# Optimization experiments

Hardware: AMD Instinct MI355X
Metric: run time of the kernel (lower is better)

The kernel has to match this reference:

```python
import jax, jax.numpy as jnp
import numpy as np

ELEM, EMBD = 512, 512

def setup_inputs() -> dict:
    key = jax.random.key(0)
    ks = jax.random.split(key, 7)
    s = 1.0 / np.sqrt(ELEM)
    return {
        "x": jax.random.normal(ks[0], (8, 2048, ELEM), dtype=jnp.float32),
        "Wq": jax.random.normal(ks[1], (ELEM, EMBD), dtype=jnp.float32) * s,
        "bq": jnp.zeros((EMBD,), dtype=jnp.float32),
        "Wk": jax.random.normal(ks[2], (ELEM, EMBD), dtype=jnp.float32) * s,
        "bk": jnp.zeros((EMBD,), dtype=jnp.float32),
        "Wv": jax.random.normal(ks[3], (ELEM, EMBD), dtype=jnp.float32) * s,
        "bv": jnp.zeros((EMBD,), dtype=jnp.float32),
    }

def reference(x, Wq, bq, Wk, bk, Wv, bv):
    # x: [N, S, E]
    q = x @ Wq + bq            # [N, S, D]
    k = x @ Wk + bk            # [N, S, D]
    v = x @ Wv + bv            # [N, S, D]
    # NOTE: original has no 1/sqrt(d) scaling.
    logits = jnp.einsum('nsd,ntd->nst', q, k)   # [N, S, S]
    attn = jax.nn.softmax(logits, axis=-1)
    return jnp.einsum('nst,ntd->nsd', attn, v)  # [N, S, D]
```

## Files before the change

kernel.cpp:

```cpp
#include <hip/hip_runtime.h>
#include <hip/hip_fp16.h>

#define SEQ 2048
#define DIM 512

typedef __attribute__((ext_vector_type(8))) short short8;
typedef __attribute__((ext_vector_type(4))) float f32x4;
typedef _Float16 h8 __attribute__((ext_vector_type(8)));
typedef _Float16 h4 __attribute__((ext_vector_type(4)));

#define MFMA16(a, b, c) __builtin_amdgcn_mfma_f32_16x16x32_f16((a), (b), (c), 0, 0, 0)

#define GLOAD_LDS16(g, l)                                                              \
    __builtin_amdgcn_global_load_lds(                                                  \
        (const __attribute__((address_space(1))) unsigned int*)(g),                    \
        (__attribute__((address_space(3))) unsigned int*)(l), 16, 0, 0)

template <int MODE>
__global__ __launch_bounds__(512, 1) void gemmw(
    const _Float16* __restrict__ A, const _Float16* __restrict__ B,
    const float* __restrict__ biasA, const float* __restrict__ biasB,
    _Float16* __restrict__ o0, _Float16* __restrict__ ovt) {
    extern __shared__ char sm[];
    constexpr int T  = (MODE == 0) ? 16 : 8;
    constexpr int PA = 512;
    constexpr int PB = (MODE == 0) ? 1024 : 512;

    int tid = threadIdx.x, wid = tid >> 6, lane = tid & 63, r = lane & 15, g = lane >> 4;
    int wm = wid >> 1, wn = wid & 1;
    int m0 = blockIdx.x * 256, n0 = blockIdx.y * 128;

    const _Float16* Ab = A + (size_t)m0 * 512;
    const _Float16* Bb = B + (size_t)n0 * PB;

    const char* gA[4];
    const char* gB[2];
    int ldsA[4], ldsB[2];
#pragma unroll
    for (int j = 0; j < 4; ++j) {
        int ci = j * 512 + tid;
        int row = ci >> 3, cl = ci & 7;
        int col16 = cl ^ (row & 7);
        gA[j] = (const char*)Ab + (size_t)row * (PA * 2) + col16 * 16;
        ldsA[j] = ci * 16;
    }
#pragma unroll
    for (int j = 0; j < 2; ++j) {
        int ci = j * 512 + tid;
        int row = ci >> 3, cl = ci & 7;
        int col16 = cl ^ (row & 7);
        gB[j] = (const char*)Bb + (size_t)row * (PB * 2) + col16 * 16;
        ldsB[j] = ci * 16;
    }
    int offA[4][2], offB[4][2];
#pragma unroll
    for (int m = 0; m < 4; ++m) {
        int rowA = wm * 64 + m * 16 + r;
        int rowB = wn * 64 + m * 16 + r;
#pragma unroll
        for (int ks = 0; ks < 2; ++ks) {
            offA[m][ks] = rowA * 128 + (((ks * 4 + g) ^ (rowA & 7)) * 16);
            offB[m][ks] = rowB * 128 + (((ks * 4 + g) ^ (rowB & 7)) * 16);
        }
    }

    f32x4 acc[4][4];
#pragma unroll
    for (int m = 0; m < 4; ++m)
#pragma unroll
        for (int n = 0; n < 4; ++n) acc[m][n] = (f32x4)(0.0f);

    auto STG = [&](int t, int b) {
        int ka = (MODE == 0) ? ((t & 7) * 128) : (t * 128);
        int kb = t * 128;
        char* dA = sm + b * 49152;
        char* dB = sm + b * 49152 + 32768;
#pragma unroll
        for (int j = 0; j < 4; ++j) GLOAD_LDS16(gA[j] + ka, dA + ldsA[j]);
#pragma unroll
        for (int j = 0; j < 2; ++j) GLOAD_LDS16(gB[j] + kb, dB + ldsB[j]);
    };

    STG(0, 0);
    STG(1, 1);
    asm volatile("s_waitcnt vmcnt(6)" ::: "memory");
    __builtin_amdgcn_s_barrier();

#pragma unroll
    for (int t = 0; t < T; ++t) {
        const int buf = t % 3;
        if (t + 2 < T) STG(t + 2, (t + 2) % 3);
        const char* bA = sm + buf * 49152;
        const char* bB = sm + buf * 49152 + 32768;
        h8 af[4][2], bf[4][2];
#pragma unroll
        for (int m = 0; m < 4; ++m)
#pragma unroll
            for (int ks = 0; ks < 2; ++ks) {
                af[m][ks] = *(const h8*)(bA + offA[m][ks]);
                bf[m][ks] = *(const h8*)(bB + offB[m][ks]);
            }
        __builtin_amdgcn_s_setprio(1);
#pragma unroll
        for (int ks = 0; ks < 2; ++ks)
#pragma unroll
            for (int m = 0; m < 4; ++m)
#pragma unroll
                for (int n = 0; n < 4; ++n)
                    acc[m][n] = MFMA16(af[m][ks], bf[n][ks], acc[m][n]);
        __builtin_amdgcn_s_setprio(0);
        if (t + 2 < T) asm volatile("s_waitcnt vmcnt(6)" ::: "memory");
        else if (t + 1 < T) asm volatile("s_waitcnt vmcnt(0)" ::: "memory");
        if (t + 1 < T) __builtin_amdgcn_s_barrier();
    }

    if (MODE == 0) {
#pragma unroll
        for (int n = 0; n < 4; ++n) {
            int col = n0 + wn * 64 + n * 16 + r;
            float bi = biasA[col];
#pragma unroll
            for (int m = 0; m < 4; ++m) {
                int grow0 = m0 + wm * 64 + m * 16 + 4 * g;
                for (int reg = 0; reg < 4; ++reg)
                    o0[(size_t)(grow0 + reg) * 512 + col] =
                        (_Float16)(acc[m][n][reg] + bi);
            }
        }
    } else {
        int p = n0 >> 9, ncl = n0 & 511;
        if (p == 0) {
#pragma unroll
            for (int n = 0; n < 4; ++n) {
                int col = ncl + wn * 64 + n * 16 + r;
                float bi = biasA[col];
#pragma unroll
                for (int m = 0; m < 4; ++m) {
                    int grow0 = m0 + wm * 64 + m * 16 + 4 * g;
                    for (int reg = 0; reg < 4; ++reg)
                        o0[(size_t)(grow0 + reg) * 512 + col] =
                            (_Float16)(acc[m][n][reg] + bi);
                }
            }
        } else {
            __syncthreads();
            _Float16* tt = (_Float16*)sm;
#pragma unroll
            for (int n = 0; n < 4; ++n) {
                int dloc = wn * 64 + n * 16 + r;
                float bi = biasB[ncl + dloc];
#pragma unroll
                for (int m = 0; m < 4; ++m) {
                    int sloc = wm * 64 + m * 16 + 4 * g;
                    h4 pv;
                    pv[0] = (_Float16)(acc[m][n][0] + bi);
                    pv[1] = (_Float16)(acc[m][n][1] + bi);
                    pv[2] = (_Float16)(acc[m][n][2] + bi);
                    pv[3] = (_Float16)(acc[m][n][3] + bi);
                    *(h4*)(&tt[dloc * 264 + sloc]) = pv;
                }
            }
            __syncthreads();
            int b = m0 >> 11, s0b = m0 & 2047;
            int drow = tid >> 2, part = tid & 3;
            const char* src = (const char*)(tt + drow * 264 + part * 64);
            char* dst = (char*)(ovt + (size_t)b * (512 * 2048) +
                                (size_t)(ncl + drow) * 2048 + s0b + part * 64);
#pragma unroll
            for (int j = 0; j < 8; ++j)
                *(short8*)(dst + j * 16) = *(const short8*)(src + j * 16);
        }
    }
}

template <int MODE>
__global__ __launch_bounds__(256) void gemmn(
    const _Float16* __restrict__ A, const _Float16* __restrict__ B,
    float* __restrict__ of, int bat0) {
    __shared__ char sm[2 * 32768];
    constexpr int T  = (MODE == 1) ? 8 : 32;
    constexpr int PA = (MODE == 1) ? 512 : 4096;
    constexpr int PB = (MODE == 1) ? 512 : 2048;

    int tid = threadIdx.x, wid = tid >> 6, lane = tid & 63, r = lane & 15, g = lane >> 4;
    int mw = wid >> 1, nw = wid & 1;
    int m0 = blockIdx.x * 128, n0 = blockIdx.y * 128, bz = blockIdx.z;

    const _Float16 *Ab, *Bb;
    if (MODE == 1) {
        int b = bat0 + bz;
        Ab = A + ((size_t)(b * SEQ) + m0) * 512;
        Bb = B + ((size_t)(b * SEQ) + n0) * 512;
    } else {
        int b = bat0 + bz;
        Ab = A + (size_t)bz * (SEQ * 4096) + (size_t)m0 * 4096;
        Bb = B + (size_t)b * (512 * SEQ) + (size_t)n0 * 2048;
    }

    const char* gA[4];
    const char* gB[4];
    int ldsw[4];
#pragma unroll
    for (int j = 0; j < 4; ++j) {
        int ci = (j * 4 + wid) * 64 + lane;
        int row = ci >> 3, cl = ci & 7;
        int col16 = cl ^ (row & 7);
        gA[j] = (const char*)Ab + (size_t)row * (PA * 2) + col16 * 16;
        gB[j] = (const char*)Bb + (size_t)row * (PB * 2) + col16 * 16;
        ldsw[j] = (j * 4 + wid) * 1024;
    }
    int offA[4][2], offB[4][2];
#pragma unroll
    for (int m = 0; m < 4; ++m) {
        int rowA = mw * 64 + m * 16 + r;
        int rowB = nw * 64 + m * 16 + r;
#pragma unroll
        for (int ks = 0; ks < 2; ++ks) {
            offA[m][ks] = rowA * 128 + (((ks * 4 + g) ^ (rowA & 7)) * 16);
            offB[m][ks] = rowB * 128 + (((ks * 4 + g) ^ (rowB & 7)) * 16);
        }
    }

    f32x4 acc[4][4];
#pragma unroll
    for (int m = 0; m < 4; ++m)
#pragma unroll
        for (int n = 0; n < 4; ++n) acc[m][n] = (f32x4)(0.0f);

    auto STG = [&](int t, int b) {
        int ka = t * 128, kb = t * 128;
        char* dA = sm + b * 32768;
        char* dB = sm + b * 32768 + 16384;
#pragma unroll
        for (int j = 0; j < 4; ++j) {
            GLOAD_LDS16(gA[j] + ka, dA + ldsw[j]);
            GLOAD_LDS16(gB[j] + kb, dB + ldsw[j]);
        }
    };

    STG(0, 0);
    asm volatile("s_waitcnt vmcnt(0)" ::: "memory");
    __builtin_amdgcn_s_barrier();

#pragma unroll
    for (int t = 0; t < T; ++t) {
        const int buf = t & 1;
        if (t + 1 < T) STG(t + 1, buf ^ 1);
        const char* bA = sm + buf * 32768;
        const char* bB = sm + buf * 32768 + 16384;
        h8 af[4][2], bf[4][2];
#pragma unroll
        for (int m = 0; m < 4; ++m)
#pragma unroll
            for (int ks = 0; ks < 2; ++ks) {
                af[m][ks] = *(const h8*)(bA + offA[m][ks]);
                bf[m][ks] = *(const h8*)(bB + offB[m][ks]);
            }
#pragma unroll
        for (int ks = 0; ks < 2; ++ks)
#pragma unroll
            for (int m = 0; m < 4; ++m)
#pragma unroll
                for (int n = 0; n < 4; ++n)
                    acc[m][n] = MFMA16(af[m][ks], bf[n][ks], acc[m][n]);
        if (t + 1 < T) {
            asm volatile("s_waitcnt vmcnt(0)" ::: "memory");
            __builtin_amdgcn_s_barrier();
        }
    }

    if (MODE == 1) {
        float* sb = of + (size_t)bz * (SEQ * (size_t)SEQ);
#pragma unroll
        for (int n = 0; n < 4; ++n) {
            int col = n0 + nw * 64 + n * 16 + r;
#pragma unroll
            for (int m = 0; m < 4; ++m) {
                int grow0 = m0 + mw * 64 + m * 16 + 4 * g;
                for (int reg = 0; reg < 4; ++reg)
                    sb[(size_t)(grow0 + reg) * SEQ + col] = acc[m][n][reg];
            }
        }
    } else {
        int b = bat0 + bz;
#pragma unroll
        for (int n = 0; n < 4; ++n) {
            int col = n0 + nw * 64 + n * 16 + r;
#pragma unroll
            for (int m = 0; m < 4; ++m) {
                int grow0 = m0 + mw * 64 + m * 16 + 4 * g;
                for (int reg = 0; reg < 4; ++reg)
                    of[(size_t)(b * SEQ + grow0 + reg) * 512 + col] = acc[m][n][reg];
            }
        }
    }
}

__global__ __launch_bounds__(256) void k0a_splitw(
    const float* __restrict__ Wq, const float* __restrict__ Wk, const float* __restrict__ Wv,
    _Float16* __restrict__ wq, _Float16* __restrict__ wkv) {
    int idx = blockIdx.x * 256 + threadIdx.x;
    int p = idx >> 18;
    int rem = idx & 262143;
    int k = rem >> 9, n = rem & 511;
    if (p == 0) {
        float w = Wq[rem];
        _Float16 h = (_Float16)w;
        wq[(size_t)n * 1024 + k] = h;
        wq[(size_t)n * 1024 + 512 + k] = (_Float16)(w - (float)h);
    } else if (p == 1) {
        wkv[(size_t)n * 512 + k] = (_Float16)Wk[rem];
    } else {
        wkv[(size_t)(512 + n) * 512 + k] = (_Float16)Wv[rem];
    }
}

__global__ __launch_bounds__(256) void k0b_splitx(
    const float* __restrict__ x, _Float16* __restrict__ xh) {
    size_t i = (size_t)(blockIdx.x * 256 + threadIdx.x) * 4;
    float4 v = *(const float4*)(x + i);
    h4 h;
    h[0] = (_Float16)v.x; h[1] = (_Float16)v.y;
    h[2] = (_Float16)v.z; h[3] = (_Float16)v.w;
    *(h4*)(xh + i) = h;
}

__global__ __launch_bounds__(256) void k3_softmax(float* __restrict__ sbuf) {
    size_t row = blockIdx.x;
    float* srow = sbuf + row * SEQ;
    int tid = threadIdx.x, lane = tid & 63, wid = tid >> 6;
    float4 v0 = *(const float4*)(srow + tid * 8);
    float4 v1 = *(const float4*)(srow + tid * 8 + 4);
    float m = fmaxf(fmaxf(fmaxf(v0.x, v0.y), fmaxf(v0.z, v0.w)),
                    fmaxf(fmaxf(v1.x, v1.y), fmaxf(v1.z, v1.w)));
    for (int d = 1; d < 64; d <<= 1) m = fmaxf(m, __shfl_xor(m, d));
    __shared__ float red1[4], red2[4];
    if (lane == 0) red1[wid] = m;
    __syncthreads();
    m = fmaxf(fmaxf(red1[0], red1[1]), fmaxf(red1[2], red1[3]));
    float e[8];
    e[0] = __expf(v0.x - m); e[1] = __expf(v0.y - m);
    e[2] = __expf(v0.z - m); e[3] = __expf(v0.w - m);
    e[4] = __expf(v1.x - m); e[5] = __expf(v1.y - m);
    e[6] = __expf(v1.z - m); e[7] = __expf(v1.w - m);
    float s = ((e[0] + e[1]) + (e[2] + e[3])) + ((e[4] + e[5]) + (e[6] + e[7]));
    for (int d = 1; d < 64; d <<= 1) s += __shfl_xor(s, d);
    if (lane == 0) red2[wid] = s;
    __syncthreads();
    s = (red2[0] + red2[1]) + (red2[2] + red2[3]);
    float inv = 1.0f / s;
    h8 ph;
    for (int j = 0; j < 8; ++j) ph[j] = (_Float16)(e[j] * inv);
    *(h8*)((char*)srow + (size_t)tid * 16) = ph;
}

extern "C" void kernel_launch(void* const* d_in, const int* in_sizes, int n_in,
                              void* d_out, int out_size, void* d_ws, size_t ws_size,
                              hipStream_t stream) {
    const float* x  = (const float*)d_in[0];
    const float* Wq = (const float*)d_in[1];
    const float* bq = (const float*)d_in[2];
    const float* Wk = (const float*)d_in[3];
    const float* bk = (const float*)d_in[4];
    const float* Wv = (const float*)d_in[5];
    const float* bv = (const float*)d_in[6];
    float* out = (float*)d_out;

    char* ws = (char*)d_ws;
    const size_t QSZ = 16777216;
    _Float16* wq  = (_Float16*)(ws);
    _Float16* wkv = (_Float16*)(ws + 1048576);
    _Float16* xh = (_Float16*)(ws + 3145728);
    _Float16* qh = (_Float16*)(ws + 3145728 + 1 * QSZ);
    _Float16* kh = (_Float16*)(ws + 3145728 + 2 * QSZ);
    _Float16* vt = (_Float16*)(ws + 3145728 + 3 * QSZ);
    const size_t sbase = 3145728 + 4 * QSZ;

    const int LDSW = 3 * 49152;
    hipFuncSetAttribute((const void*)gemmw<0>,
                        hipFuncAttributeMaxDynamicSharedMemorySize, LDSW);
    hipFuncSetAttribute((const void*)gemmw<1>,
                        hipFuncAttributeMaxDynamicSharedMemorySize, LDSW);

    k0a_splitw<<<3072, 256, 0, stream>>>(Wq, Wk, Wv, wq, wkv);
    k0b_splitx<<<8192, 256, 0, stream>>>(x, xh);
    gemmw<0><<<dim3(64, 4), 512, LDSW, stream>>>(xh, wq, bq, nullptr, qh, nullptr);
    gemmw<1><<<dim3(64, 8), 512, LDSW, stream>>>(xh, wkv, bk, bv, kh, vt);

    size_t avail = (ws_size > sbase) ? (ws_size - sbase) : 0;
    int chunk = (int)(avail / QSZ);
    if (chunk < 1) chunk = 1;
    if (chunk > 8) chunk = 8;
    float* sc = (float*)(ws + sbase);
    for (int b0 = 0; b0 < 8; b0 += chunk) {
        int nb = (8 - b0 < chunk) ? (8 - b0) : chunk;
        gemmn<1><<<dim3(16, 16, nb), 256, 0, stream>>>(qh, kh, sc, b0);
        k3_softmax<<<dim3(nb * SEQ), 256, 0, stream>>>(sc);
        gemmn<2><<<dim3(16, 4, nb), 256, 0, stream>>>((const _Float16*)sc, vt, out, b0);
    }
}
```

Before: 174.1 us.

## Remap block indices for XCD locality and move PV GEMM to larger-tile kernel

Flattens the grids and remaps block IDs so that consecutive blocks on the same XCD share A-row tiles, improving L2 reuse across the chiplets. The attention-times-V GEMM now runs in the 512-thread, 256x128-tile gemmw kernel (new MODE 2) instead of the 128x128 gemmn kernel, which raises operand reuse per block. The cost is fewer blocks for the PV GEMM (nb*32), which may underfill the 256 CUs, and the remapping assumes round-robin block-to-XCD dispatch.

```diff
diff --git a/kernel.cpp b/kernel.cpp
--- a/kernel.cpp
+++ b/kernel.cpp
@@ -20,18 +20,30 @@
 __global__ __launch_bounds__(512, 1) void gemmw(
     const _Float16* __restrict__ A, const _Float16* __restrict__ B,
     const float* __restrict__ biasA, const float* __restrict__ biasB,
-    _Float16* __restrict__ o0, _Float16* __restrict__ ovt) {
+    _Float16* __restrict__ o0, _Float16* __restrict__ ovt,
+    float* __restrict__ ofp, int bat0) {
     extern __shared__ char sm[];
-    constexpr int T  = (MODE == 0) ? 16 : 8;
-    constexpr int PA = 512;
-    constexpr int PB = (MODE == 0) ? 1024 : 512;
+    constexpr int T  = (MODE == 0) ? 16 : (MODE == 1) ? 8 : 32;
+    constexpr int PA = (MODE == 2) ? 4096 : 512;
+    constexpr int PB = (MODE == 0) ? 1024 : (MODE == 1) ? 512 : 2048;
 
     int tid = threadIdx.x, wid = tid >> 6, lane = tid & 63, r = lane & 15, g = lane >> 4;
     int wm = wid >> 1, wn = wid & 1;
-    int m0 = blockIdx.x * 256, n0 = blockIdx.y * 128;
-
-    const _Float16* Ab = A + (size_t)m0 * 512;
-    const _Float16* Bb = B + (size_t)n0 * PB;
+    int L = blockIdx.x, xcd = L & 7, s = L >> 3;
+    int m0, n0, bz = 0;
+    if (MODE == 0)      { m0 = (xcd * 8 + (s >> 2)) * 256; n0 = (s & 3) * 128; }
+    else if (MODE == 1) { m0 = (xcd * 8 + (s >> 3)) * 256; n0 = (s & 7) * 128; }
+    else                { m0 = xcd * 256; bz = s >> 2; n0 = (s & 3) * 128; }
+
+    const _Float16 *Ab, *Bb;
+    if (MODE == 2) {
+        int b = bat0 + bz;
+        Ab = A + (size_t)bz * (SEQ * 4096) + (size_t)m0 * 4096;
+        Bb = B + (size_t)b * (512 * SEQ) + (size_t)n0 * 2048;
+    } else {
+        Ab = A + (size_t)m0 * 512;
+        Bb = B + (size_t)n0 * PB;
+    }
 
     const char* gA[4];
     const char* gB[2];
@@ -127,7 +139,7 @@
                         (_Float16)(acc[m][n][reg] + bi);
             }
         }
-    } else {
+    } else if (MODE == 1) {
         int p = n0 >> 9, ncl = n0 & 511;
         if (p == 0) {
 #pragma unroll
@@ -170,32 +182,38 @@
             for (int j = 0; j < 8; ++j)
                 *(short8*)(dst + j * 16) = *(const short8*)(src + j * 16);
         }
-    }
-}
-
-template <int MODE>
-__global__ __launch_bounds__(256) void gemmn(
+    } else {
+        int b = bat0 + bz;
+#pragma unroll
+        for (int n = 0; n < 4; ++n) {
+            int col = n0 + wn * 64 + n * 16 + r;
+#pragma unroll
+            for (int m = 0; m < 4; ++m) {
+                int grow0 = m0 + wm * 64 + m * 16 + 4 * g;
+                for (int reg = 0; reg < 4; ++reg)
+                    ofp[(size_t)(b * SEQ + grow0 + reg) * 512 + col] = acc[m][n][reg];
+            }
+        }
+    }
+}
+
+__global__ __launch_bounds__(256) void gemmn_qk(
     const _Float16* __restrict__ A, const _Float16* __restrict__ B,
     float* __restrict__ of, int bat0) {
     __shared__ char sm[2 * 32768];
-    constexpr int T  = (MODE == 1) ? 8 : 32;
-    constexpr int PA = (MODE == 1) ? 512 : 4096;
-    constexpr int PB = (MODE == 1) ? 512 : 2048;
+    constexpr int T = 8, PA = 512, PB = 512;
 
     int tid = threadIdx.x, wid = tid >> 6, lane = tid & 63, r = lane & 15, g = lane >> 4;
     int mw = wid >> 1, nw = wid & 1;
-    int m0 = blockIdx.x * 128, n0 = blockIdx.y * 128, bz = blockIdx.z;
-
-    const _Float16 *Ab, *Bb;
-    if (MODE == 1) {
-        int b = bat0 + bz;
-        Ab = A + ((size_t)(b * SEQ) + m0) * 512;
-        Bb = B + ((size_t)(b * SEQ) + n0) * 512;
-    } else {
-        int b = bat0 + bz;
-        Ab = A + (size_t)bz * (SEQ * 4096) + (size_t)m0 * 4096;
-        Bb = B + (size_t)b * (512 * SEQ) + (size_t)n0 * 2048;
-    }
+    int L = blockIdx.x, xcd = L & 7, s = L >> 3;
+    int bz = s >> 5;
+    int rem = s & 31;
+    int m0 = (xcd * 2 + (rem >> 4)) * 128;
+    int n0 = (rem & 15) * 128;
+
+    int b = bat0 + bz;
+    const _Float16* Ab = A + ((size_t)(b * SEQ) + m0) * 512;
+    const _Float16* Bb = B + ((size_t)(b * SEQ) + n0) * 512;
 
     const char* gA[4];
     const char* gB[4];
@@ -227,10 +245,10 @@
 #pragma unroll
         for (int n = 0; n < 4; ++n) acc[m][n] = (f32x4)(0.0f);
 
-    auto STG = [&](int t, int b) {
+    auto STG = [&](int t, int bb) {
         int ka = t * 128, kb = t * 128;
-        char* dA = sm + b * 32768;
-        char* dB = sm + b * 32768 + 16384;
+        char* dA = sm + bb * 32768;
+        char* dB = sm + bb * 32768 + 16384;
 #pragma unroll
         for (int j = 0; j < 4; ++j) {
             GLOAD_LDS16(gA[j] + ka, dA + ldsw[j]);
@@ -269,60 +287,17 @@
         }
     }
 
-    if (MODE == 1) {
-        float* sb = of + (size_t)bz * (SEQ * (size_t)SEQ);
-#pragma unroll
-        for (int n = 0; n < 4; ++n) {
-            int col = n0 + nw * 64 + n * 16 + r;
-#pragma unroll
-            for (int m = 0; m < 4; ++m) {
-                int grow0 = m0 + mw * 64 + m * 16 + 4 * g;
-                for (int reg = 0; reg < 4; ++reg)
-                    sb[(size_t)(grow0 + reg) * SEQ + col] = acc[m][n][reg];
-            }
-        }
-    } else {
-        int b = bat0 + bz;
-#pragma unroll
-        for (int n = 0; n < 4; ++n) {
-            int col = n0 + nw * 64 + n * 16 + r;
-#pragma unroll
-            for (int m = 0; m < 4; ++m) {
-                int grow0 = m0 + mw * 64 + m * 16 + 4 * g;
-                for (int reg = 0; reg < 4; ++reg)
-                    of[(size_t)(b * SEQ + grow0 + reg) * 512 + col] = acc[m][n][reg];
-            }
-        }
-    }
-}
-
-__global__ __launch_bounds__(256) void k0a_splitw(
-    const float* __restrict__ Wq, const float* __restrict__ Wk, const float* __restrict__ Wv,
-    _Float16* __restrict__ wq, _Float16* __restrict__ wkv) {
-    int idx = blockIdx.x * 256 + threadIdx.x;
-    int p = idx >> 18;
-    int rem = idx & 262143;
-    int k = rem >> 9, n = rem & 511;
-    if (p == 0) {
-        float w = Wq[rem];
-        _Float16 h = (_Float16)w;
-        wq[(size_t)n * 1024 + k] = h;
-        wq[(size_t)n * 1024 + 512 + k] = (_Float16)(w - (float)h);
-    } else if (p == 1) {
-        wkv[(size_t)n * 512 + k] = (_Float16)Wk[rem];
-    } else {
-        wkv[(size_t)(512 + n) * 512 + k] = (_Float16)Wv[rem];
-    }
-}
-
-__global__ __launch_bounds__(256) void k0b_splitx(
-    const float* __restrict__ x, _Float16* __restrict__ xh) {
-    size_t i = (size_t)(blockIdx.x * 256 + threadIdx.x) * 4;
-    float4 v = *(const float4*)(x + i);
-    h4 h;
-    h[0] = (_Float16)v.x; h[1] = (_Float16)v.y;
-    h[2] = (_Float16)v.z; h[3] = (_Float16)v.w;
-    *(h4*)(xh + i) = h;
+    float* sb = of + (size_t)bz * (SEQ * (size_t)SEQ);
+#pragma unroll
+    for (int n = 0; n < 4; ++n) {
+        int col = n0 + nw * 64 + n * 16 + r;
+#pragma unroll
+        for (int m = 0; m < 4; ++m) {
+            int grow0 = m0 + mw * 64 + m * 16 + 4 * g;
+            for (int reg = 0; reg < 4; ++reg)
+                sb[(size_t)(grow0 + reg) * SEQ + col] = acc[m][n][reg];
+        }
+    }
 }
 
 __global__ __launch_bounds__(256) void k3_softmax(float* __restrict__ sbuf) {
@@ -354,6 +329,35 @@
     *(h8*)((char*)srow + (size_t)tid * 16) = ph;
 }
 
+__global__ __launch_bounds__(256) void k0a_splitw(
+    const float* __restrict__ Wq, const float* __restrict__ Wk, const float* __restrict__ Wv,
+    _Float16* __restrict__ wq, _Float16* __restrict__ wkv) {
+    int idx = blockIdx.x * 256 + threadIdx.x;
+    int p = idx >> 18;
+    int rem = idx & 262143;
+    int k = rem >> 9, n = rem & 511;
+    if (p == 0) {
+        float w = Wq[rem];
+        _Float16 h = (_Float16)w;
+        wq[(size_t)n * 1024 + k] = h;
+        wq[(size_t)n * 1024 + 512 + k] = (_Float16)(w - (float)h);
+    } else if (p == 1) {
+        wkv[(size_t)n * 512 + k] = (_Float16)Wk[rem];
+    } else {
+        wkv[(size_t)(512 + n) * 512 + k] = (_Float16)Wv[rem];
+    }
+}
+
+__global__ __launch_bounds__(256) void k0b_splitx(
+    const float* __restrict__ x, _Float16* __restrict__ xh) {
+    size_t i = (size_t)(blockIdx.x * 256 + threadIdx.x) * 4;
+    float4 v = *(const float4*)(x + i);
+    h4 h;
+    h[0] = (_Float16)v.x; h[1] = (_Float16)v.y;
+    h[2] = (_Float16)v.z; h[3] = (_Float16)v.w;
+    *(h4*)(xh + i) = h;
+}
+
 extern "C" void kernel_launch(void* const* d_in, const int* in_sizes, int n_in,
                               void* d_out, int out_size, void* d_ws, size_t ws_size,
                               hipStream_t stream) {
@@ -381,11 +385,14 @@
                         hipFuncAttributeMaxDynamicSharedMemorySize, LDSW);
     hipFuncSetAttribute((const void*)gemmw<1>,
                         hipFuncAttributeMaxDynamicSharedMemorySize, LDSW);
+    hipFuncSetAttribute((const void*)gemmw<2>,
+                        hipFuncAttributeMaxDynamicSharedMemorySize, LDSW);
 
     k0a_splitw<<<3072, 256, 0, stream>>>(Wq, Wk, Wv, wq, wkv);
     k0b_splitx<<<8192, 256, 0, stream>>>(x, xh);
-    gemmw<0><<<dim3(64, 4), 512, LDSW, stream>>>(xh, wq, bq, nullptr, qh, nullptr);
-    gemmw<1><<<dim3(64, 8), 512, LDSW, stream>>>(xh, wkv, bk, bv, kh, vt);
+    gemmw<0><<<256, 512, LDSW, stream>>>(xh, wq, bq, nullptr, qh, nullptr,
+                                         nullptr, 0);
+    gemmw<1><<<512, 512, LDSW, stream>>>(xh, wkv, bk, bv, kh, vt, nullptr, 0);
 
     size_t avail = (ws_size > sbase) ? (ws_size - sbase) : 0;
     int chunk = (int)(avail / QSZ);
@@ -394,8 +401,10 @@
     float* sc = (float*)(ws + sbase);
     for (int b0 = 0; b0 < 8; b0 += chunk) {
         int nb = (8 - b0 < chunk) ? (8 - b0) : chunk;
-        gemmn<1><<<dim3(16, 16, nb), 256, 0, stream>>>(qh, kh, sc, b0);
+        gemmn_qk<<<nb * 256, 256, 0, stream>>>(qh, kh, sc, b0);
         k3_softmax<<<dim3(nb * SEQ), 256, 0, stream>>>(sc);
-        gemmn<2><<<dim3(16, 4, nb), 256, 0, stream>>>((const _Float16*)sc, vt, out, b0);
-    }
-}
+        gemmw<2><<<nb * 32, 512, LDSW, stream>>>((const _Float16*)sc, vt,
+                                                 nullptr, nullptr, nullptr,
+                                                 nullptr, out, b0);
+    }
+}
```

After: 173.1 us. No clear change (-0.6%).
